# Kernel optimization log

Hardware: AMD Instinct MI355X
Metric: run time of the kernel (lower is better)

## Reference

```python
import jax, jax.numpy as jnp
import numpy as np

T, U, I, B, K = 64, 142, 4500, 16384, 10


def setup_inputs() -> dict:
    key = jax.random.key(0)
    k1, k2, k3, k4, k5, k6 = jax.random.split(key, 6)
    q = jax.random.uniform(k1, (T, U, I), dtype=jnp.float32, minval=0.01, maxval=5.0)
    miss = jax.random.uniform(k2, (T, U, I)) < 0.3
    qos_tensor = jnp.where(miss, 0.0, q)
    # user_avg exactly as in __init__: sum over items / count of rated items (clamped >= 1)
    cnt = jnp.clip((qos_tensor > 0).sum(axis=2).astype(jnp.float32), 1.0, None)
    user_avg = qos_tensor.sum(axis=2) / cnt  # [T, U]
    # time-aggregated similarity: random symmetric matrix in [-1, 1]
    s = jax.random.uniform(k3, (U, U), dtype=jnp.float32, minval=-1.0, maxval=1.0)
    user_sim_agg = 0.5 * (s + s.T)
    user_id = jax.random.randint(k4, (B,), 0, U)
    item_id = jax.random.randint(k5, (B,), 0, I)
    time_id = jax.random.randint(k6, (B,), 0, T)
    return {
        "qos_tensor": qos_tensor,
        "user_avg": user_avg,
        "user_sim_agg": user_sim_agg,
        "user_id": user_id,
        "item_id": item_id,
        "time_id": time_id,
        "top_k": K,
    }


def reference(qos_tensor, user_avg, user_sim_agg, user_id, item_id, time_id, top_k):
    num_users = qos_tensor.shape[1]
    avg_u = user_avg[time_id, user_id]                      # [B]
    sim_u = user_sim_agg[user_id]                           # [B, U]
    # ratings of every user for (time_id, item_id): column gather, [B, U]
    u_idx = jnp.arange(num_users)[None, :]
    item_col = qos_tensor[time_id[:, None], u_idx, item_id[:, None]]
    item_rated = item_col > 0                               # [B, U]
    sim_m = jnp.where(item_rated, sim_u, 0.0)
    top_sim, top_user = jax.lax.top_k(sim_m, top_k)         # [B, K]
    top_sim = top_sim / (top_sim.sum(axis=1, keepdims=True) + 1e-8)
    top_sim = jnp.nan_to_num(top_sim)
    # neighbor ratings and neighbor averages
    r_vs = qos_tensor[time_id[:, None], top_user, item_id[:, None]]  # [B, K]
    avg_v = user_avg[time_id[:, None], top_user]                     # [B, K]
    pred = avg_u + (top_sim * (r_vs - avg_v)).sum(axis=1)            # [B]
    return pred
```

## Files before the change

kernel.cpp:

```cpp
#include <hip/hip_runtime.h>
#include <math.h>

#define T_DIM 64
#define U_DIM 142
#define I_DIM 4500
#define B_DIM 16384
#define K_TOP 10

__global__ __launch_bounds__(256) void ucf_kernel(
    const float* __restrict__ qos,
    const float* __restrict__ user_avg,
    const float* __restrict__ user_sim,
    const int*   __restrict__ user_id,
    const int*   __restrict__ item_id,
    const int*   __restrict__ time_id,
    float*       __restrict__ out)
{
    const int lane = threadIdx.x & 63;
    const int wid  = threadIdx.x >> 6;
    const int b    = blockIdx.x * 4 + wid;
    if (b >= B_DIM) return;

    const int u = user_id[b];
    const int i = item_id[b];
    const int t = time_id[b];

    const float* qcol = qos + ((size_t)t * U_DIM) * (size_t)I_DIM + i;
    const float* srow = user_sim + (size_t)u * U_DIM;
    const float* arow = user_avg + (size_t)t * U_DIM;

    float val[3];
    float con[3];
#pragma unroll
    for (int j = 0; j < 3; ++j) {
        const int v = lane + j * 64;
        float sv = -INFINITY;
        float cv = 0.0f;
        if (v < U_DIM) {
            const float rv = qcol[(size_t)v * I_DIM];
            const float av = arow[v];
            const float s  = srow[v];
            sv = (rv > 0.0f) ? s : 0.0f;
            cv = sv * (rv - av);
        }
        val[j] = sv;
        con[j] = cv;
    }

    float ssum = 0.0f;
    float wsum = 0.0f;
#pragma unroll
    for (int k = 0; k < K_TOP; ++k) {
        float mv = val[0]; float mc = con[0]; int mk = lane;
        if (val[1] > mv) { mv = val[1]; mc = con[1]; mk = lane + 64; }
        if (val[2] > mv) { mv = val[2]; mc = con[2]; mk = lane + 128; }
#pragma unroll
        for (int off = 32; off > 0; off >>= 1) {
            const float ov = __shfl_xor(mv, off, 64);
            const float oc = __shfl_xor(mc, off, 64);
            const int   ok = __shfl_xor(mk, off, 64);
            if (ov > mv || (ov == mv && ok < mk)) { mv = ov; mc = oc; mk = ok; }
        }
        ssum += mv;
        wsum += mc;
        if ((mk & 63) == lane) {
            const int slot = mk >> 6;
            if (slot == 0)      val[0] = -INFINITY;
            else if (slot == 1) val[1] = -INFINITY;
            else                val[2] = -INFINITY;
        }
    }

    if (lane == 0) {
        const float avg_u = arow[u];
        out[b] = avg_u + wsum / (ssum + 1e-8f);
    }
}

extern "C" void kernel_launch(void* const* d_in, const int* in_sizes, int n_in,
                              void* d_out, int out_size, void* d_ws, size_t ws_size,
                              hipStream_t stream) {
    const float* qos  = (const float*)d_in[0];
    const float* uavg = (const float*)d_in[1];
    const float* usim = (const float*)d_in[2];
    const int*   uid  = (const int*)d_in[3];
    const int*   iid  = (const int*)d_in[4];
    const int*   tid  = (const int*)d_in[5];
    float* out = (float*)d_out;

    dim3 block(256);
    dim3 grid(B_DIM / 4);
    ucf_kernel<<<grid, block, 0, stream>>>(qos, uavg, usim, uid, iid, tid, out);
}
```

Measured before the change: 247.1 us.

## Precompute per-item rated-user bitmask, then select top-k from compact mask

Adds a pre-pass kernel that streams the whole QoS tensor once, coalesced as float4 loads, and writes a 5-word bitmask per (time, item) marking which users rated it. The selection kernel then reads the 20-byte mask instead of 142 strided column loads. It gathers ratings and averages only for the 10 chosen neighbours, spread one per lane, and sums them with shuffles. This trades latency-bound scattered gathers for one full bandwidth-bound pass over the tensor on every call. It also relies on a workspace buffer being provided, and falls back to the old kernel if none is.

```diff
diff --git a/kernel.cpp b/kernel.cpp
--- a/kernel.cpp
+++ b/kernel.cpp
@@ -6,6 +6,129 @@
 #define I_DIM 4500
 #define B_DIM 16384
 #define K_TOP 10
+
+#define NWPC  5
+#define NCH   18
+#define MASK_INTS ((size_t)T_DIM * I_DIM * NWPC)
+#define WS_BYTES  (MASK_INTS * sizeof(unsigned))
+
+__global__ __launch_bounds__(256) void build_mask(
+    const float* __restrict__ qos,
+    unsigned*    __restrict__ mask)
+{
+    const int lane = threadIdx.x & 63;
+    const int gw   = blockIdx.x * 4 + (threadIdx.x >> 6);
+    const int w    = gw % NWPC;
+    const int tc   = gw / NWPC;
+    const int c    = tc % NCH;
+    const int t    = tc / NCH;
+
+    const int i0 = c * 256 + lane * 4;
+    if (i0 + 3 >= I_DIM) return;
+
+    const int v0 = w * 32;
+    const int nv = (w == 4) ? (U_DIM - 128) : 32;
+
+    const float* p = qos + ((size_t)t * U_DIM + v0) * I_DIM + i0;
+    unsigned m0 = 0, m1 = 0, m2 = 0, m3 = 0;
+#pragma unroll 4
+    for (int k = 0; k < nv; ++k, p += I_DIM) {
+        const float4 q = *(const float4*)p;
+        const unsigned bit = 1u << ((v0 + k) & 31);
+        if (q.x > 0.0f) m0 |= bit;
+        if (q.y > 0.0f) m1 |= bit;
+        if (q.z > 0.0f) m2 |= bit;
+        if (q.w > 0.0f) m3 |= bit;
+    }
+    unsigned* mp = mask + ((size_t)t * I_DIM + i0) * NWPC + w;
+    mp[0 * NWPC] = m0;
+    mp[1 * NWPC] = m1;
+    mp[2 * NWPC] = m2;
+    mp[3 * NWPC] = m3;
+}
+
+__global__ __launch_bounds__(256) void ucf_select(
+    const float*    __restrict__ qos,
+    const float*    __restrict__ user_avg,
+    const float*    __restrict__ user_sim,
+    const int*      __restrict__ user_id,
+    const int*      __restrict__ item_id,
+    const int*      __restrict__ time_id,
+    const unsigned* __restrict__ mask,
+    float*          __restrict__ out)
+{
+    const int lane = threadIdx.x & 63;
+    const int wid  = threadIdx.x >> 6;
+    const int b    = blockIdx.x * 4 + wid;
+    if (b >= B_DIM) return;
+
+    const int u = user_id[b];
+    const int i = item_id[b];
+    const int t = time_id[b];
+
+    const unsigned* mp = mask + ((size_t)t * I_DIM + i) * NWPC;
+    const unsigned mw = (lane < NWPC) ? mp[lane] : 0u;
+
+    const float* srow = user_sim + (size_t)u * U_DIM;
+    const float* arow = user_avg + (size_t)t * U_DIM;
+
+    const unsigned wA = __shfl(mw, lane >> 5, 64);
+    const unsigned wB = __shfl(mw, 2 + (lane >> 5), 64);
+    const unsigned wC = __shfl(mw, 4, 64);
+    const unsigned bitm = 1u << (lane & 31);
+
+    float val0 = (wA & bitm) ? srow[lane] : 0.0f;
+    float val1 = (wB & bitm) ? srow[lane + 64] : 0.0f;
+    float val2 = -INFINITY;
+    const bool has2 = (lane + 128) < U_DIM;
+    if (has2) val2 = (wC & bitm) ? srow[lane + 128] : 0.0f;
+
+    float ssum = 0.0f;
+    float wv[K_TOP];
+    int   wk[K_TOP];
+#pragma unroll
+    for (int k = 0; k < K_TOP; ++k) {
+        float mv = val0; int mk = lane;
+        if (val1 > mv) { mv = val1; mk = lane + 64; }
+        if (val2 > mv) { mv = val2; mk = lane + 128; }
+#pragma unroll
+        for (int off = 32; off > 0; off >>= 1) {
+            const float ov = __shfl_xor(mv, off, 64);
+            const int   ok = __shfl_xor(mk, off, 64);
+            if (ov > mv || (ov == mv && ok < mk)) { mv = ov; mk = ok; }
+        }
+        wv[k] = mv;
+        wk[k] = mk;
+        ssum += mv;
+        const int sl = mk >> 6;
+        const int wl = mk & 63;
+        if (wl == lane) {
+            if (sl == 0)      val0 = -INFINITY;
+            else if (sl == 1) val1 = -INFINITY;
+            else              val2 = -INFINITY;
+        }
+    }
+
+    float myval = 0.0f; int myv = -1;
+#pragma unroll
+    for (int k = 0; k < K_TOP; ++k)
+        if (lane == k) { myv = wk[k]; myval = wv[k]; }
+
+    float c = 0.0f;
+    if (myv >= 0) {
+        const float rv = qos[((size_t)t * U_DIM + (size_t)myv) * I_DIM + i];
+        const float av = arow[myv];
+        c = myval * (rv - av);
+    }
+
+    float wsum = 0.0f;
+#pragma unroll
+    for (int k = 0; k < K_TOP; ++k)
+        wsum += __shfl(c, k, 64);
+
+    if (lane == 0)
+        out[b] = arow[u] + wsum / (ssum + 1e-8f);
+}
 
 __global__ __launch_bounds__(256) void ucf_kernel(
     const float* __restrict__ qos,
@@ -47,8 +170,7 @@
         con[j] = cv;
     }
 
-    float ssum = 0.0f;
-    float wsum = 0.0f;
+    float ssum = 0.0f, wsum = 0.0f;
 #pragma unroll
     for (int k = 0; k < K_TOP; ++k) {
         float mv = val[0]; float mc = con[0]; int mk = lane;
@@ -72,8 +194,7 @@
     }
 
     if (lane == 0) {
-        const float avg_u = arow[u];
-        out[b] = avg_u + wsum / (ssum + 1e-8f);
+        out[b] = arow[u] + wsum / (ssum + 1e-8f);
     }
 }
 
@@ -88,7 +209,13 @@
     const int*   tid  = (const int*)d_in[5];
     float* out = (float*)d_out;
 
-    dim3 block(256);
-    dim3 grid(B_DIM / 4);
-    ucf_kernel<<<grid, block, 0, stream>>>(qos, uavg, usim, uid, iid, tid, out);
-}
+    if (d_ws != nullptr && ws_size >= WS_BYTES) {
+        unsigned* mask = (unsigned*)d_ws;
+        build_mask<<<dim3(T_DIM * NCH * NWPC / 4), dim3(256), 0, stream>>>(qos, mask);
+        ucf_select<<<dim3(B_DIM / 4), dim3(256), 0, stream>>>(
+            qos, uavg, usim, uid, iid, tid, mask, out);
+    } else {
+        ucf_kernel<<<dim3(B_DIM / 4), dim3(256), 0, stream>>>(
+            qos, uavg, usim, uid, iid, tid, out);
+    }
+}
```

After: 269.5 us. +9.1%, slower.

## Sort queries by (time, 64B item line) bucket to improve gather cache reuse

Applied to the files above, without the earlier changes.

Adds a counting-sort preprocessing pipeline (zero counts, atomic bin count, single-block scan, scatter) that orders batch queries by time step and 16-item line before the main gather kernel. Neighboring wavefronts then touch the same qos cache lines, so strided column gathers are meant to hit L2/MALL instead of HBM. In exchange it adds four extra kernel launches, including a serial single-block scan, and falls back to the old kernel when no workspace is available.

```diff
diff --git a/kernel.cpp b/kernel.cpp
--- a/kernel.cpp
+++ b/kernel.cpp
@@ -7,19 +7,84 @@
 #define B_DIM 16384
 #define K_TOP 10
 
-__global__ __launch_bounds__(256) void ucf_kernel(
+#define NILINE 282
+#define NCELL2 (T_DIM * NILINE)
+
+#define CNT_OFF    0
+#define BASE_OFF   (NCELL2)
+#define MYSLOT_OFF (2 * NCELL2)
+#define PERM_OFF   (2 * NCELL2 + B_DIM)
+#define WS_INTS    (2 * NCELL2 + 2 * B_DIM)
+#define WS_BYTES   ((size_t)WS_INTS * sizeof(int))
+
+__global__ void zero_cnt(int* __restrict__ ws)
+{
+    const int k = blockIdx.x * 256 + threadIdx.x;
+    if (k < NCELL2) ws[CNT_OFF + k] = 0;
+}
+
+__global__ __launch_bounds__(256) void bin_count(
+    const int* __restrict__ time_id,
+    const int* __restrict__ item_id,
+    int*       __restrict__ ws)
+{
+    const int b = blockIdx.x * 256 + threadIdx.x;
+    if (b >= B_DIM) return;
+    const int cell = time_id[b] * NILINE + (item_id[b] >> 4);
+    ws[MYSLOT_OFF + b] = atomicAdd(&ws[CNT_OFF + cell], 1);
+}
+
+__global__ __launch_bounds__(1024) void scan_cells(int* __restrict__ ws)
+{
+    __shared__ int s[1024];
+    const int tid = threadIdx.x;
+    const int n0 = tid * 18;
+    int n1 = n0 + 18; if (n1 > NCELL2) n1 = NCELL2;
+
+    int lsum = 0;
+    for (int k = n0; k < n1; ++k) lsum += ws[CNT_OFF + k];
+    s[tid] = lsum;
+    __syncthreads();
+
+    for (int off = 1; off < 1024; off <<= 1) {
+        const int t = (tid >= off) ? s[tid - off] : 0;
+        __syncthreads();
+        s[tid] += t;
+        __syncthreads();
+    }
+    int run = s[tid] - lsum;
+    for (int k = n0; k < n1; ++k) {
+        ws[BASE_OFF + k] = run;
+        run += ws[CNT_OFF + k];
+    }
+}
+
+__global__ __launch_bounds__(256) void scatter_perm(
+    const int* __restrict__ time_id,
+    const int* __restrict__ item_id,
+    int*       __restrict__ ws)
+{
+    const int b = blockIdx.x * 256 + threadIdx.x;
+    if (b >= B_DIM) return;
+    const int cell = time_id[b] * NILINE + (item_id[b] >> 4);
+    ws[PERM_OFF + ws[BASE_OFF + cell] + ws[MYSLOT_OFF + b]] = b;
+}
+
+__global__ __launch_bounds__(256) void ucf_final(
     const float* __restrict__ qos,
     const float* __restrict__ user_avg,
     const float* __restrict__ user_sim,
     const int*   __restrict__ user_id,
     const int*   __restrict__ item_id,
     const int*   __restrict__ time_id,
+    const int*   __restrict__ ws,
     float*       __restrict__ out)
 {
     const int lane = threadIdx.x & 63;
     const int wid  = threadIdx.x >> 6;
-    const int b    = blockIdx.x * 4 + wid;
-    if (b >= B_DIM) return;
+    const int slot = blockIdx.x * 4 + wid;
+    if (slot >= B_DIM) return;
+    const int b = ws[PERM_OFF + slot];
 
     const int u = user_id[b];
     const int i = item_id[b];
@@ -47,8 +112,7 @@
         con[j] = cv;
     }
 
-    float ssum = 0.0f;
-    float wsum = 0.0f;
+    float ssum = 0.0f, wsum = 0.0f;
 #pragma unroll
     for (int k = 0; k < K_TOP; ++k) {
         float mv = val[0]; float mc = con[0]; int mk = lane;
@@ -64,16 +128,83 @@
         ssum += mv;
         wsum += mc;
         if ((mk & 63) == lane) {
-            const int slot = mk >> 6;
-            if (slot == 0)      val[0] = -INFINITY;
-            else if (slot == 1) val[1] = -INFINITY;
-            else                val[2] = -INFINITY;
+            const int sl = mk >> 6;
+            if (sl == 0)      val[0] = -INFINITY;
+            else if (sl == 1) val[1] = -INFINITY;
+            else              val[2] = -INFINITY;
         }
     }
 
     if (lane == 0) {
-        const float avg_u = arow[u];
-        out[b] = avg_u + wsum / (ssum + 1e-8f);
+        out[b] = arow[u] + wsum / (ssum + 1e-8f);
+    }
+}
+
+__global__ __launch_bounds__(256) void ucf_kernel(
+    const float* __restrict__ qos,
+    const float* __restrict__ user_avg,
+    const float* __restrict__ user_sim,
+    const int*   __restrict__ user_id,
+    const int*   __restrict__ item_id,
+    const int*   __restrict__ time_id,
+    float*       __restrict__ out)
+{
+    const int lane = threadIdx.x & 63;
+    const int wid  = threadIdx.x >> 6;
+    const int b    = blockIdx.x * 4 + wid;
+    if (b >= B_DIM) return;
+
+    const int u = user_id[b];
+    const int i = item_id[b];
+    const int t = time_id[b];
+
+    const float* qcol = qos + ((size_t)t * U_DIM) * (size_t)I_DIM + i;
+    const float* srow = user_sim + (size_t)u * U_DIM;
+    const float* arow = user_avg + (size_t)t * U_DIM;
+
+    float val[3];
+    float con[3];
+#pragma unroll
+    for (int j = 0; j < 3; ++j) {
+        const int v = lane + j * 64;
+        float sv = -INFINITY;
+        float cv = 0.0f;
+        if (v < U_DIM) {
+            const float rv = qcol[(size_t)v * I_DIM];
+            const float av = arow[v];
+            const float s  = srow[v];
+            sv = (rv > 0.0f) ? s : 0.0f;
+            cv = sv * (rv - av);
+        }
+        val[j] = sv;
+        con[j] = cv;
+    }
+
+    float ssum = 0.0f, wsum = 0.0f;
+#pragma unroll
+    for (int k = 0; k < K_TOP; ++k) {
+        float mv = val[0]; float mc = con[0]; int mk = lane;
+        if (val[1] > mv) { mv = val[1]; mc = con[1]; mk = lane + 64; }
+        if (val[2] > mv) { mv = val[2]; mc = con[2]; mk = lane + 128; }
+#pragma unroll
+        for (int off = 32; off > 0; off >>= 1) {
+            const float ov = __shfl_xor(mv, off, 64);
+            const float oc = __shfl_xor(mc, off, 64);
+            const int   ok = __shfl_xor(mk, off, 64);
+            if (ov > mv || (ov == mv && ok < mk)) { mv = ov; mc = oc; mk = ok; }
+        }
+        ssum += mv;
+        wsum += mc;
+        if ((mk & 63) == lane) {
+            const int sl = mk >> 6;
+            if (sl == 0)      val[0] = -INFINITY;
+            else if (sl == 1) val[1] = -INFINITY;
+            else              val[2] = -INFINITY;
+        }
+    }
+
+    if (lane == 0) {
+        out[b] = arow[u] + wsum / (ssum + 1e-8f);
     }
 }
 
@@ -88,7 +219,16 @@
     const int*   tid  = (const int*)d_in[5];
     float* out = (float*)d_out;
 
-    dim3 block(256);
-    dim3 grid(B_DIM / 4);
-    ucf_kernel<<<grid, block, 0, stream>>>(qos, uavg, usim, uid, iid, tid, out);
-}
+    if (d_ws != nullptr && ws_size >= WS_BYTES) {
+        int* ws = (int*)d_ws;
+        zero_cnt<<<dim3((NCELL2 + 255) / 256), dim3(256), 0, stream>>>(ws);
+        bin_count<<<dim3(B_DIM / 256), dim3(256), 0, stream>>>(tid, iid, ws);
+        scan_cells<<<dim3(1), dim3(1024), 0, stream>>>(ws);
+        scatter_perm<<<dim3(B_DIM / 256), dim3(256), 0, stream>>>(tid, iid, ws);
+        ucf_final<<<dim3(B_DIM / 4), dim3(256), 0, stream>>>(
+            qos, uavg, usim, uid, iid, tid, ws, out);
+    } else {
+        ucf_kernel<<<dim3(B_DIM / 4), dim3(256), 0, stream>>>(
+            qos, uavg, usim, uid, iid, tid, out);
+    }
+}
```

After: 271.4 us. 9.9% more time.
